# Optimization experiments

Measured on AMD Instinct MI355X. Metric: run time of the kernel, lower is better.

Reference implementation:

```python
import jax, jax.numpy as jnp
import numpy as np

B, T, D, H, E, TOP_K = 2, 2048, 1024, 4096, 8, 2


def setup_inputs() -> dict:
    key = jax.random.key(0)
    ks = jax.random.split(key, 7)
    s_d = 1.0 / np.sqrt(D)
    s_h = 1.0 / np.sqrt(H)
    return {
        "x": jax.random.normal(ks[0], (B, T, D), dtype=jnp.float32),
        "gate_w": jax.random.uniform(ks[1], (D, E), minval=-s_d, maxval=s_d, dtype=jnp.float32),
        "gate_b": jax.random.uniform(ks[2], (E,), minval=-s_d, maxval=s_d, dtype=jnp.float32),
        "w1": jax.random.uniform(ks[3], (E, D, H), minval=-s_d, maxval=s_d, dtype=jnp.float32),
        "b1": jax.random.uniform(ks[4], (E, H), minval=-s_d, maxval=s_d, dtype=jnp.float32),
        "w2": jax.random.uniform(ks[5], (E, H, D), minval=-s_h, maxval=s_h, dtype=jnp.float32),
        "b2": jax.random.uniform(ks[6], (E, D), minval=-s_h, maxval=s_h, dtype=jnp.float32),
    }


def reference(x, gate_w, gate_b, w1, b1, w2, b2):
    Bsz, Tn, Din = x.shape
    x_flat = x.reshape(-1, Din)                       # [N, D]
    N = x_flat.shape[0]
    gating_logits = x_flat @ gate_w + gate_b          # [N, E]
    weights, indices = jax.lax.top_k(gating_logits, TOP_K)
    weights = jax.nn.softmax(weights, axis=-1).astype(x.dtype)
    # scatter top-k weights into dense dispatch tensor [N, E]
    dispatch = jnp.zeros((N, E), dtype=x.dtype).at[jnp.arange(N)[:, None], indices].set(weights)
    # NOTE: faithful to original - gate weight multiplies the expert INPUT
    # and again the expert OUTPUT (double weighting through the GELU MLP).
    dispatched_x = dispatch[:, :, None] * x_flat[:, None, :]       # [N, E, D]
    h = jax.nn.gelu(jnp.einsum('ned,edh->neh', dispatched_x, w1) + b1, approximate=False)
    expert_out = jnp.einsum('neh,ehd->ned', h, w2) + b2            # [N, E, D]
    combined = jnp.sum(dispatch[:, :, None] * expert_out, axis=1)  # [N, D]
    final = combined.reshape(Bsz, Tn, -1)
    return final, gating_logits
```

## Files before the change

kernel.cpp:

```cpp
#include <hip/hip_runtime.h>
#include <hip/hip_bf16.h>
#include <math.h>

#define NTOK 4096
#define DDIM 1024
#define HDIM 4096
#define NEXP 8
#define CAP  4096
#define ROWCAP 10240
#define MAXTILES 40

typedef __attribute__((ext_vector_type(8))) short short8;
typedef __attribute__((ext_vector_type(4))) float f32x4;

#define GLOAD_LDS16(g, l) __builtin_amdgcn_global_load_lds( \
    (const __attribute__((address_space(1))) void*)(g),     \
    (__attribute__((address_space(3))) void*)(l), 16, 0, 0)

__global__ __launch_bounds__(256) void gating_kernel(
    const float* __restrict__ x, const float* __restrict__ gw,
    const float* __restrict__ gb, float* __restrict__ logits_out,
    int* __restrict__ counts, int* __restrict__ tok, float* __restrict__ gate,
    int* __restrict__ eA, int* __restrict__ sA, float* __restrict__ gA) {
  int t = blockIdx.x;
  int tid = threadIdx.x;
  float p[NEXP];
#pragma unroll
  for (int e = 0; e < NEXP; ++e) p[e] = 0.f;
  const float* xr = x + (size_t)t * DDIM;
  for (int d = tid; d < DDIM; d += 256) {
    float xv = xr[d];
    const float* wr = gw + (size_t)d * NEXP;
#pragma unroll
    for (int e = 0; e < NEXP; ++e) p[e] += xv * wr[e];
  }
#pragma unroll
  for (int off = 32; off > 0; off >>= 1)
#pragma unroll
    for (int e = 0; e < NEXP; ++e) p[e] += __shfl_xor(p[e], off, 64);
  __shared__ float red[4][NEXP];
  int wave = tid >> 6, lane = tid & 63;
  if (lane == 0)
#pragma unroll
    for (int e = 0; e < NEXP; ++e) red[wave][e] = p[e];
  __syncthreads();
  if (tid < NEXP) {
    float v = red[0][tid] + red[1][tid] + red[2][tid] + red[3][tid] + gb[tid];
    logits_out[(size_t)t * NEXP + tid] = v;
    red[0][tid] = v;
  }
  __syncthreads();
  if (tid == 0) {
    float v[NEXP];
#pragma unroll
    for (int e = 0; e < NEXP; ++e) v[e] = red[0][e];
    int i0 = 0;
#pragma unroll
    for (int e = 1; e < NEXP; ++e) if (v[e] > v[i0]) i0 = e;
    int i1 = (i0 == 0) ? 1 : 0;
#pragma unroll
    for (int e = 0; e < NEXP; ++e) if (e != i0 && v[e] > v[i1]) i1 = e;
    float e1 = expf(v[i1] - v[i0]);
    float s = 1.f + e1;
    float g0 = 1.f / s, g1 = e1 / s;
    int s0 = atomicAdd(&counts[i0], 1);
    tok[i0 * CAP + s0] = t; gate[i0 * CAP + s0] = g0;
    int s1 = atomicAdd(&counts[i1], 1);
    tok[i1 * CAP + s1] = t; gate[i1 * CAP + s1] = g1;
    eA[2 * t] = i0; sA[2 * t] = s0; gA[2 * t] = g0;
    eA[2 * t + 1] = i1; sA[2 * t + 1] = s1; gA[2 * t + 1] = g1;
  }
}

__global__ void sched_kernel(const int* __restrict__ counts, int* __restrict__ poff,
                             int* __restrict__ tileE, int* __restrict__ tileR,
                             int* __restrict__ nTiles) {
  if (threadIdx.x == 0) {
    int acc = 0, nt = 0;
    for (int e = 0; e < NEXP; ++e) {
      poff[e] = acc;
      int tl = (counts[e] + 255) >> 8;
      for (int t = 0; t < tl; ++t) { tileE[nt] = e; tileR[nt] = acc + t * 256; ++nt; }
      acc += tl << 8;
    }
    poff[NEXP] = acc;
    nTiles[0] = nt;
  }
}

__global__ __launch_bounds__(256) void transpose_all(
    const float* __restrict__ w1, const float* __restrict__ w2,
    __hip_bfloat16* __restrict__ wT1, __hip_bfloat16* __restrict__ wT2) {
  __shared__ float tile[64 * 65];
  int id = blockIdx.x;
  const float* inp; __hip_bfloat16* outp; int R, C, bx, by;
  if (id < 8192) {
    int e = id >> 10, rem = id & 1023;
    bx = rem & 63; by = rem >> 6;
    R = 1024; C = 4096;
    inp = w1 + (size_t)e * R * C; outp = wT1 + (size_t)e * R * C;
  } else {
    id -= 8192;
    int e = id >> 10, rem = id & 1023;
    bx = rem & 15; by = rem >> 4;
    R = 4096; C = 1024;
    inp = w2 + (size_t)e * R * C; outp = wT2 + (size_t)e * R * C;
  }
  int c0 = bx * 64, r0 = by * 64;
  int tx = threadIdx.x & 15, ty = threadIdx.x >> 4;
#pragma unroll
  for (int i = 0; i < 64; i += 16) {
    float4 v = *(const float4*)(inp + (size_t)(r0 + ty + i) * C + c0 + tx * 4);
    float* dst = tile + (ty + i) * 65 + tx * 4;
    dst[0] = v.x; dst[1] = v.y; dst[2] = v.z; dst[3] = v.w;
  }
  __syncthreads();
  int c = threadIdx.x >> 3;
  int rb = (threadIdx.x & 7) * 8;
#pragma unroll
  for (int p = 0; p < 2; ++p) {
    int cc = c + p * 32;
    union { unsigned short u[8]; short8 v8; } pk;
#pragma unroll
    for (int j = 0; j < 8; ++j) {
      __hip_bfloat16 h = __float2bfloat16(tile[(rb + j) * 65 + cc]);
      pk.u[j] = *(unsigned short*)&h;
    }
    *(short8*)(outp + (size_t)(c0 + cc) * R + r0 + rb) = pk.v8;
  }
}

__global__ __launch_bounds__(256) void gather_kernel(
    const float* __restrict__ x, const int* __restrict__ counts,
    const int* __restrict__ poff, const int* __restrict__ tok,
    const float* __restrict__ gate, __hip_bfloat16* __restrict__ Xg) {
  int e = blockIdx.y, r = blockIdx.x;
  int pc = poff[e + 1] - poff[e];
  if (r >= pc) return;
  int row = poff[e] + r;
  int tid = threadIdx.x;
  __hip_bfloat16* orow = Xg + (size_t)row * DDIM;
  if (r < counts[e]) {
    int t = tok[e * CAP + r];
    float g = gate[e * CAP + r];
    float4 v = ((const float4*)(x + (size_t)t * DDIM))[tid];
    union { unsigned short u[4]; uint2 q; } pk;
    __hip_bfloat16 h0 = __float2bfloat16(v.x * g);
    __hip_bfloat16 h1 = __float2bfloat16(v.y * g);
    __hip_bfloat16 h2 = __float2bfloat16(v.z * g);
    __hip_bfloat16 h3 = __float2bfloat16(v.w * g);
    pk.u[0] = *(unsigned short*)&h0; pk.u[1] = *(unsigned short*)&h1;
    pk.u[2] = *(unsigned short*)&h2; pk.u[3] = *(unsigned short*)&h3;
    ((uint2*)orow)[tid] = pk.q;
  } else {
    uint2 z; z.x = 0; z.y = 0;
    ((uint2*)orow)[tid] = z;
  }
}

template <int EPI>
__global__ __launch_bounds__(512) void moe_gemm(
    const __hip_bfloat16* __restrict__ A, const __hip_bfloat16* __restrict__ B,
    const float* __restrict__ bias, __hip_bfloat16* __restrict__ Hout,
    float* __restrict__ Pout, const int* __restrict__ tileE,
    const int* __restrict__ tileR, const int* __restrict__ nTiles,
    int K, int Nn) {
  int f = (blockIdx.z * gridDim.y + blockIdx.y) * gridDim.x + blockIdx.x;
  int xcd = f & 7, seq = f >> 3;
  int ct, ty, kz;
  if (EPI == 0) {
    ct = xcd * 4 + (seq & 3); ty = seq >> 2; kz = 0;
  } else {
    ct = xcd; ty = seq % MAXTILES; kz = seq / MAXTILES;
  }
  if (ty >= nTiles[0]) return;
  int e = tileE[ty];
  int rowBase = tileR[ty];
  int colBase = ct * 128;

  __shared__ __align__(16) char LA[65536];
  __shared__ __align__(16) char LB[32768];

  const char* Ae = (const char*)A + (size_t)rowBase * K * 2;
  const char* Be = (const char*)B + ((size_t)e * Nn + colBase) * (size_t)K * 2;

  int tid = threadIdx.x;
  int lane = tid & 63, wave = tid >> 6;
  int wm = (wave >> 1) * 64, wn = (wave & 1) * 64;
  int frm = lane & 15, g = lane >> 4;

  int sr = tid >> 3;
  int sch = (tid & 7) ^ (sr & 7);
  const char* aS = Ae + (size_t)sr * K * 2 + sch * 16;
  const char* bS = Be + (size_t)sr * K * 2 + sch * 16;
  char* dA = LA + tid * 16;
  char* dB = LB + tid * 16;
  size_t rstep = (size_t)64 * K * 2;

  int f7 = frm & 7;
  int sl0 = (g ^ f7) << 4;
  int sl1 = ((4 + g) ^ f7) << 4;
  const char* rA = LA + (wm + frm) * 128;
  const char* rB = LB + (wn + frm) * 128;

  f32x4 acc[4][4] = {};
  int kPer = (EPI == 1) ? (K >> 1) : K;
  int kLo = kz * kPer;
  int NT = kPer >> 6;

  {
    const char* a = aS + (size_t)kLo * 2;
    const char* b = bS + (size_t)kLo * 2;
#pragma unroll
    for (int j = 0; j < 4; ++j) GLOAD_LDS16(a + j * rstep, dA + j * 8192);
#pragma unroll
    for (int j = 0; j < 2; ++j) GLOAD_LDS16(b + j * rstep, dB + j * 8192);
  }
  asm volatile("s_waitcnt vmcnt(0)" ::: "memory");
  __builtin_amdgcn_sched_barrier(0);
  __builtin_amdgcn_s_barrier();

  for (int t = 0; t < NT; ++t) {
    int p = t & 1;
    if (t + 1 < NT) {
      const char* a = aS + (size_t)(kLo + (t + 1) * 64) * 2;
      const char* b = bS + (size_t)(kLo + (t + 1) * 64) * 2;
      char* da = dA + (p ^ 1) * 32768;
      char* db = dB + (p ^ 1) * 16384;
#pragma unroll
      for (int j = 0; j < 4; ++j) GLOAD_LDS16(a + j * rstep, da + j * 8192);
#pragma unroll
      for (int j = 0; j < 2; ++j) GLOAD_LDS16(b + j * rstep, db + j * 8192);
    }
    const char* Ab = rA + p * 32768;
    const char* Bb = rB + p * 16384;
    short8 af[2][2], bf[4][2], ag[2][2];
#pragma unroll
    for (int i = 0; i < 2; ++i) {
      af[i][0] = *(const short8*)(Ab + i * 2048 + sl0);
      af[i][1] = *(const short8*)(Ab + i * 2048 + sl1);
    }
#pragma unroll
    for (int j = 0; j < 4; ++j) {
      bf[j][0] = *(const short8*)(Bb + j * 2048 + sl0);
      bf[j][1] = *(const short8*)(Bb + j * 2048 + sl1);
    }
    __builtin_amdgcn_s_barrier();
    asm volatile("s_waitcnt lgkmcnt(0)" ::: "memory");
    __builtin_amdgcn_sched_barrier(0);
    __builtin_amdgcn_s_setprio(1);
#pragma unroll
    for (int ks = 0; ks < 2; ++ks)
#pragma unroll
      for (int i = 0; i < 2; ++i)
#pragma unroll
        for (int j = 0; j < 4; ++j)
          acc[i][j] = __builtin_amdgcn_mfma_f32_16x16x32_bf16(
              af[i][ks], bf[j][ks], acc[i][j], 0, 0, 0);
    __builtin_amdgcn_s_setprio(0);
    __builtin_amdgcn_s_barrier();
#pragma unroll
    for (int i = 0; i < 2; ++i) {
      ag[i][0] = *(const short8*)(Ab + (i + 2) * 2048 + sl0);
      ag[i][1] = *(const short8*)(Ab + (i + 2) * 2048 + sl1);
    }
    __builtin_amdgcn_s_barrier();
    asm volatile("s_waitcnt lgkmcnt(0)" ::: "memory");
    __builtin_amdgcn_sched_barrier(0);
    __builtin_amdgcn_s_setprio(1);
#pragma unroll
    for (int ks = 0; ks < 2; ++ks)
#pragma unroll
      for (int i = 0; i < 2; ++i)
#pragma unroll
        for (int j = 0; j < 4; ++j)
          acc[i + 2][j] = __builtin_amdgcn_mfma_f32_16x16x32_bf16(
              ag[i][ks], bf[j][ks], acc[i + 2][j], 0, 0, 0);
    __builtin_amdgcn_s_setprio(0);
    asm volatile("s_waitcnt vmcnt(0)" ::: "memory");
    __builtin_amdgcn_sched_barrier(0);
    __builtin_amdgcn_s_barrier();
  }

  int cq = lane >> 4, cn = lane & 15;
  if (EPI == 0) {
#pragma unroll
    for (int i = 0; i < 4; ++i) {
#pragma unroll
      for (int j = 0; j < 4; ++j) {
        int col = colBase + wn + j * 16 + cn;
        float bv = bias[e * Nn + col];
#pragma unroll
        for (int r = 0; r < 4; ++r) {
          int row = rowBase + wm + i * 16 + cq * 4 + r;
          float v = acc[i][j][r] + bv;
          float z = 1.5957691f * v * (1.0f + 0.044715f * v * v);
          v = v / (1.0f + __expf(-z));
          Hout[(size_t)row * Nn + col] = __float2bfloat16(v);
        }
      }
    }
  } else {
    float* Pp = Pout + ((size_t)kz * ROWCAP + rowBase) * DDIM;
#pragma unroll
    for (int i = 0; i < 4; ++i) {
#pragma unroll
      for (int j = 0; j < 4; ++j) {
        int col = colBase + wn + j * 16 + cn;
#pragma unroll
        for (int r = 0; r < 4; ++r) {
          int row = wm + i * 16 + cq * 4 + r;
          Pp[(size_t)row * DDIM + col] = acc[i][j][r];
        }
      }
    }
  }
}

__global__ __launch_bounds__(256) void combine_kernel(
    const float* __restrict__ P, const float* __restrict__ b2,
    const int* __restrict__ poff, const int* __restrict__ eA,
    const int* __restrict__ sA, const float* __restrict__ gA,
    float* __restrict__ outF) {
  int t = blockIdx.x, c = threadIdx.x;
  int e0 = eA[2 * t], e1 = eA[2 * t + 1];
  int r0 = poff[e0] + sA[2 * t], r1 = poff[e1] + sA[2 * t + 1];
  float g0 = gA[2 * t], g1 = gA[2 * t + 1];
  float4 a0 = ((const float4*)(P + (size_t)r0 * DDIM))[c];
  float4 a1 = ((const float4*)(P + ((size_t)ROWCAP + r0) * DDIM))[c];
  float4 b0 = ((const float4*)(P + (size_t)r1 * DDIM))[c];
  float4 b1 = ((const float4*)(P + ((size_t)ROWCAP + r1) * DDIM))[c];
  float4 bb0 = ((const float4*)(b2 + (size_t)e0 * DDIM))[c];
  float4 bb1 = ((const float4*)(b2 + (size_t)e1 * DDIM))[c];
  float4 o;
  o.x = g0 * (a0.x + a1.x + bb0.x) + g1 * (b0.x + b1.x + bb1.x);
  o.y = g0 * (a0.y + a1.y + bb0.y) + g1 * (b0.y + b1.y + bb1.y);
  o.z = g0 * (a0.z + a1.z + bb0.z) + g1 * (b0.z + b1.z + bb1.z);
  o.w = g0 * (a0.w + a1.w + bb0.w) + g1 * (b0.w + b1.w + bb1.w);
  ((float4*)(outF + (size_t)t * DDIM))[c] = o;
}

extern "C" void kernel_launch(void* const* d_in, const int* in_sizes, int n_in,
                              void* d_out, int out_size, void* d_ws, size_t ws_size,
                              hipStream_t stream) {
  const float* x  = (const float*)d_in[0];
  const float* gw = (const float*)d_in[1];
  const float* gb = (const float*)d_in[2];
  const float* w1 = (const float*)d_in[3];
  const float* b1 = (const float*)d_in[4];
  const float* w2 = (const float*)d_in[5];
  const float* b2 = (const float*)d_in[6];

  float* outF = (float*)d_out;
  float* outL = outF + (size_t)NTOK * DDIM;

  size_t off = 0;
  char* base = (char*)d_ws;
  auto alloc = [&](size_t bytes) {
    void* r = base + off;
    off += (bytes + 255) & ~(size_t)255;
    return r;
  };
  __hip_bfloat16* wT1 = (__hip_bfloat16*)alloc((size_t)NEXP * HDIM * DDIM * 2);
  __hip_bfloat16* Xg  = (__hip_bfloat16*)alloc((size_t)ROWCAP * DDIM * 2);
  __hip_bfloat16* wT2 = (__hip_bfloat16*)alloc((size_t)NEXP * DDIM * HDIM * 2);
  __hip_bfloat16* Hact= (__hip_bfloat16*)alloc((size_t)ROWCAP * HDIM * 2);
  int*   tok    = (int*)alloc((size_t)NEXP * CAP * 4);
  float* gate   = (float*)alloc((size_t)NEXP * CAP * 4);
  int*   eA     = (int*)alloc((size_t)NTOK * 2 * 4);
  int*   sA     = (int*)alloc((size_t)NTOK * 2 * 4);
  float* gA     = (float*)alloc((size_t)NTOK * 2 * 4);
  int*   counts = (int*)alloc(64);
  int*   poff   = (int*)alloc(64);
  int*   tileE  = (int*)alloc(MAXTILES * 4);
  int*   tileR  = (int*)alloc(MAXTILES * 4);
  int*   nTiles = (int*)alloc(64);
  float* P      = (float*)wT1;

  hipMemsetAsync(counts, 0, 64, stream);
  gating_kernel<<<NTOK, 256, 0, stream>>>(x, gw, gb, outL, counts, tok, gate, eA, sA, gA);
  sched_kernel<<<1, 64, 0, stream>>>(counts, poff, tileE, tileR, nTiles);
  transpose_all<<<16384, 256, 0, stream>>>(w1, w2, wT1, wT2);
  gather_kernel<<<dim3(CAP, NEXP), 256, 0, stream>>>(x, counts, poff, tok, gate, Xg);
  moe_gemm<0><<<dim3(HDIM / 128, MAXTILES, 1), 512, 0, stream>>>(
      Xg, wT1, b1, Hact, nullptr, tileE, tileR, nTiles, DDIM, HDIM);
  moe_gemm<1><<<dim3(DDIM / 128, MAXTILES, 2), 512, 0, stream>>>(
      Hact, wT2, b2, nullptr, P, tileE, tileR, nTiles, HDIM, DDIM);
  combine_kernel<<<NTOK, 256, 0, stream>>>(P, b2, poff, eA, sA, gA, outF);
}
```

Before: 760.9 us.

## Triple-buffer LDS tiles and merge MFMA phases in expert GEMM

Switches the expert GEMM main loop from double to triple buffering of A/B tiles in LDS, prefetching two k-steps ahead and waiting only for the oldest batch of async loads (vmcnt(6)). It also merges the two half-tile MFMA phases into one, loading all four A fragments at once and dropping two of the per-iteration barriers. The aim is to hide global load latency and cut synchronisation. In exchange it uses 144KB of LDS per block, which limits occupancy to one block per CU, and raises register pressure from holding more fragments.

```diff
diff --git a/kernel.cpp b/kernel.cpp
--- a/kernel.cpp
+++ b/kernel.cpp
@@ -178,8 +178,8 @@
   int rowBase = tileR[ty];
   int colBase = ct * 128;
 
-  __shared__ __align__(16) char LA[65536];
-  __shared__ __align__(16) char LB[32768];
+  __shared__ __align__(16) char LA[98304];
+  __shared__ __align__(16) char LB[49152];
 
   const char* Ae = (const char*)A + (size_t)rowBase * K * 2;
   const char* Be = (const char*)B + ((size_t)e * Nn + colBase) * (size_t)K * 2;
@@ -207,79 +207,70 @@
   int kPer = (EPI == 1) ? (K >> 1) : K;
   int kLo = kz * kPer;
   int NT = kPer >> 6;
-
-  {
-    const char* a = aS + (size_t)kLo * 2;
-    const char* b = bS + (size_t)kLo * 2;
-#pragma unroll
-    for (int j = 0; j < 4; ++j) GLOAD_LDS16(a + j * rstep, dA + j * 8192);
-#pragma unroll
-    for (int j = 0; j < 2; ++j) GLOAD_LDS16(b + j * rstep, dB + j * 8192);
-  }
-  asm volatile("s_waitcnt vmcnt(0)" ::: "memory");
+  const char* aP = aS + (size_t)kLo * 2;
+  const char* bP = bS + (size_t)kLo * 2;
+
+#pragma unroll
+  for (int tt = 0; tt < 2; ++tt) {
+    const char* a = aP + tt * 128;
+    const char* b = bP + tt * 128;
+    char* da = dA + tt * 32768;
+    char* db = dB + tt * 16384;
+#pragma unroll
+    for (int j = 0; j < 4; ++j) GLOAD_LDS16(a + j * rstep, da + j * 8192);
+#pragma unroll
+    for (int j = 0; j < 2; ++j) GLOAD_LDS16(b + j * rstep, db + j * 8192);
+  }
+  asm volatile("s_waitcnt vmcnt(6)" ::: "memory");
   __builtin_amdgcn_sched_barrier(0);
   __builtin_amdgcn_s_barrier();
 
+  int rbuf = 0, nbuf = 2;
   for (int t = 0; t < NT; ++t) {
-    int p = t & 1;
-    if (t + 1 < NT) {
-      const char* a = aS + (size_t)(kLo + (t + 1) * 64) * 2;
-      const char* b = bS + (size_t)(kLo + (t + 1) * 64) * 2;
-      char* da = dA + (p ^ 1) * 32768;
-      char* db = dB + (p ^ 1) * 16384;
+    if (t + 2 < NT) {
+      const char* a = aP + (size_t)(t + 2) * 128;
+      const char* b = bP + (size_t)(t + 2) * 128;
+      char* da = dA + nbuf * 32768;
+      char* db = dB + nbuf * 16384;
 #pragma unroll
       for (int j = 0; j < 4; ++j) GLOAD_LDS16(a + j * rstep, da + j * 8192);
 #pragma unroll
       for (int j = 0; j < 2; ++j) GLOAD_LDS16(b + j * rstep, db + j * 8192);
     }
-    const char* Ab = rA + p * 32768;
-    const char* Bb = rB + p * 16384;
-    short8 af[2][2], bf[4][2], ag[2][2];
-#pragma unroll
-    for (int i = 0; i < 2; ++i) {
+    const char* Ab = rA + rbuf * 32768;
+    const char* Bb = rB + rbuf * 16384;
+    short8 af[4][2], bfr[4][2];
+#pragma unroll
+    for (int i = 0; i < 4; ++i) {
       af[i][0] = *(const short8*)(Ab + i * 2048 + sl0);
       af[i][1] = *(const short8*)(Ab + i * 2048 + sl1);
     }
 #pragma unroll
     for (int j = 0; j < 4; ++j) {
-      bf[j][0] = *(const short8*)(Bb + j * 2048 + sl0);
-      bf[j][1] = *(const short8*)(Bb + j * 2048 + sl1);
-    }
-    __builtin_amdgcn_s_barrier();
+      bfr[j][0] = *(const short8*)(Bb + j * 2048 + sl0);
+      bfr[j][1] = *(const short8*)(Bb + j * 2048 + sl1);
+    }
     asm volatile("s_waitcnt lgkmcnt(0)" ::: "memory");
     __builtin_amdgcn_sched_barrier(0);
     __builtin_amdgcn_s_setprio(1);
 #pragma unroll
     for (int ks = 0; ks < 2; ++ks)
 #pragma unroll
-      for (int i = 0; i < 2; ++i)
+      for (int i = 0; i < 4; ++i)
 #pragma unroll
         for (int j = 0; j < 4; ++j)
           acc[i][j] = __builtin_amdgcn_mfma_f32_16x16x32_bf16(
-              af[i][ks], bf[j][ks], acc[i][j], 0, 0, 0);
+              af[i][ks], bfr[j][ks], acc[i][j], 0, 0, 0);
     __builtin_amdgcn_s_setprio(0);
-    __builtin_amdgcn_s_barrier();
-#pragma unroll
-    for (int i = 0; i < 2; ++i) {
-      ag[i][0] = *(const short8*)(Ab + (i + 2) * 2048 + sl0);
-      ag[i][1] = *(const short8*)(Ab + (i + 2) * 2048 + sl1);
-    }
-    __builtin_amdgcn_s_barrier();
-    asm volatile("s_waitcnt lgkmcnt(0)" ::: "memory");
-    __builtin_amdgcn_sched_barrier(0);
-    __builtin_amdgcn_s_setprio(1);
-#pragma unroll
-    for (int ks = 0; ks < 2; ++ks)
-#pragma unroll
-      for (int i = 0; i < 2; ++i)
-#pragma unroll
-        for (int j = 0; j < 4; ++j)
-          acc[i + 2][j] = __builtin_amdgcn_mfma_f32_16x16x32_bf16(
-              ag[i][ks], bf[j][ks], acc[i + 2][j], 0, 0, 0);
-    __builtin_amdgcn_s_setprio(0);
-    asm volatile("s_waitcnt vmcnt(0)" ::: "memory");
+    if (t + 2 < NT) {
+      asm volatile("s_waitcnt vmcnt(6)" ::: "memory");
+    } else {
+      asm volatile("s_waitcnt vmcnt(0)" ::: "memory");
+    }
     __builtin_amdgcn_sched_barrier(0);
     __builtin_amdgcn_s_barrier();
+    rbuf = (rbuf + 1 == 3) ? 0 : rbuf + 1;
+    nbuf = (nbuf + 1 == 3) ? 0 : nbuf + 1;
   }
 
   int cq = lane >> 4, cn = lane & 15;
```

Result: faster. 739.4 us (-2.8%).
